# Optimization experiments

Hardware: AMD Instinct MI355X
Metric: run time of the kernel (lower is better)

Reference implementation:

```python
import jax, jax.numpy as jnp
import numpy as np

N_NODES = 50000


def setup_inputs() -> dict:
    key = jax.random.key(0)
    ks = jax.random.split(key, 8)
    d_in, d_h, d_out = 128, 128, 1
    s_in = 1.0 / np.sqrt(d_in)
    s_h = 1.0 / np.sqrt(d_h)
    return {
        "x": jax.random.normal(ks[0], (N_NODES, d_in), dtype=jnp.float32),
        "edge_index": jax.random.randint(ks[1], (2, 800000), 0, N_NODES, dtype=jnp.int64),
        "W1a": jax.random.normal(ks[2], (d_in, d_h), dtype=jnp.float32) * s_in,
        "b1a": jnp.zeros((d_h,), dtype=jnp.float32),
        "W1b": jax.random.normal(ks[3], (d_h, d_h), dtype=jnp.float32) * s_h,
        "b1b": jnp.zeros((d_h,), dtype=jnp.float32),
        "W2a": jax.random.normal(ks[4], (d_h, d_h), dtype=jnp.float32) * s_h,
        "b2a": jnp.zeros((d_h,), dtype=jnp.float32),
        "W2b": jax.random.normal(ks[5], (d_h, d_h), dtype=jnp.float32) * s_h,
        "b2b": jnp.zeros((d_h,), dtype=jnp.float32),
        "Wfc": jax.random.normal(ks[6], (d_h, d_out), dtype=jnp.float32) * s_h,
        "bfc": jnp.zeros((d_out,), dtype=jnp.float32),
    }


def _gin_conv(x, src, dst, Wa, ba, Wb, bb):
    # GINConv (eps=0): h_i = MLP((1+eps)*x_i + sum_{j->i} x_j)
    agg = jax.ops.segment_sum(x[src], dst, num_segments=N_NODES)
    h = x + agg
    h = jax.nn.relu(h @ Wa + ba)
    h = jax.nn.relu(h @ Wb + bb)
    return h


def reference(x, edge_index, W1a, b1a, W1b, b1b, W2a, b2a, W2b, b2b, Wfc, bfc):
    src, dst = edge_index[0], edge_index[1]
    h = _gin_conv(x, src, dst, W1a, b1a, W1b, b1b)
    h = _gin_conv(h, src, dst, W2a, b2a, W2b, b2b)
    out = h @ Wfc + bfc
    return jax.nn.sigmoid(out)
```

## Files before the change

### kernel.cpp

```cpp
#include <hip/hip_runtime.h>
#include <hip/hip_fp16.h>
#include <cstdint>
#include <cstddef>

#define D 128
#define NP 8
#define S_CSR 96
typedef __attribute__((ext_vector_type(8))) _Float16 half8;
typedef __attribute__((ext_vector_type(4))) float f32x4;
typedef __attribute__((ext_vector_type(4))) uint uint4n;

__device__ __forceinline__ uint pack2h(float x, float y) {
    __half2 h = __floats2half2_rn(x, y);
    return *(uint*)&h;
}
__device__ __forceinline__ __half2 u2h(uint u) { return *(__half2*)&u; }
__device__ __forceinline__ uint h2u(__half2 h) { return *(uint*)&h; }
__device__ __forceinline__ int pad16(int v) { return (v + 15) & ~15; }

__global__ __launch_bounds__(256) void prep(const float* __restrict__ x,
                                            uint* __restrict__ X32,
                                            const float* __restrict__ W0,
                                            const float* __restrict__ W1,
                                            const float* __restrict__ W2,
                                            const float* __restrict__ W3,
                                            ushort* __restrict__ P0,
                                            ushort* __restrict__ P1,
                                            ushort* __restrict__ P2,
                                            ushort* __restrict__ P3,
                                            int* __restrict__ cnt,
                                            const unsigned int* __restrict__ ei,
                                            int* __restrict__ flag,
                                            uint* __restrict__ zrow0,
                                            uint* __restrict__ zrow2,
                                            ushort* __restrict__ csr,
                                            int M, int cvtB, int mB) {
    int b = blockIdx.x, t = threadIdx.x;
    if (b < cvtB) {
        long long gid = (long long)b * 256 + t;
        if (gid >= (long long)M * 16) return;
        int node = (int)(gid >> 4), q = (int)(gid & 15);
        const float4* xp = (const float4*)(x + (size_t)node * D + q * 8);
        float4 v0 = xp[0], v1 = xp[1];
        uint4n o;
        o.x = pack2h(v0.x, v0.y); o.y = pack2h(v0.z, v0.w);
        o.z = pack2h(v1.x, v1.y); o.w = pack2h(v1.z, v1.w);
        ((uint4n*)X32)[(size_t)node * 16 + q] = o;
    } else if (b < cvtB + 256) {
        int o = ((b - cvtB) & 63) * 256 + t;
        int which = (b - cvtB) >> 6;
        const float* W = which == 0 ? W0 : which == 1 ? W1 : which == 2 ? W2 : W3;
        ushort* P = which == 0 ? P0 : which == 1 ? P1 : which == 2 ? P2 : P3;
        int j = o & 7, g = (o >> 3) & 3, n = (o >> 5) & 127, ks = o >> 12;
        int k = ks * 32 + g * 8 + j;
        __half h = __float2half_rn(W[k * 128 + n]);
        P[o] = *(ushort*)&h;
    } else if (b < cvtB + 256 + mB) {
        int i = (b - cvtB - 256) * 256 + t;
        if (i < M) cnt[i] = 0;
        if (b == cvtB + 256 && t < 64) {
            zrow0[(size_t)M * 64 + t] = 0u;
            zrow2[(size_t)M * 64 + t] = 0u;
            if (t == 0) {
                int is64 = (ei[1] == 0u && ei[3] == 0u && ei[5] == 0u && ei[7] == 0u) ? 1 : 0;
                *flag = is64;
            }
        }
    } else {
        long long idx = (long long)(b - cvtB - 256 - mB) * 256 + t;
        long long tot = (long long)M * (S_CSR / 2);
        uint sv = (uint)M | ((uint)M << 16);
        if (idx < tot) ((uint*)csr)[idx] = sv;
    }
}

__global__ __launch_bounds__(256) void fill_csr_part(const void* __restrict__ ei,
                                                     const int* __restrict__ flag,
                                                     int* __restrict__ cnt,
                                                     ushort* __restrict__ csr,
                                                     int E, int M, int nslice) {
    int p = blockIdx.x & (NP - 1);
    int slice = blockIdx.x >> 3;
    int psz = (M + NP - 1) / NP;
    int lo = p * psz, hi = min(M, lo + psz);
    int eps = (E + nslice - 1) / nslice;
    int e0 = slice * eps, e1 = min(E, e0 + eps);
    int sh = *flag;
    const int* sp = (const int*)ei;
    const int* dp = sp + ((long long)E << sh);
    for (int e = e0 + threadIdx.x; e < e1; e += 256) {
        int d = dp[e << sh];
        if (d >= lo && d < hi) {
            int s = sp[e << sh];
            int pos = atomicAdd(&cnt[d], 1);
            if (pos < S_CSR) csr[(size_t)d * S_CSR + pos] = (ushort)s;
        }
    }
}

__global__ __launch_bounds__(256) void aggregate_f16(const uint* __restrict__ X,
                                                     const int* __restrict__ cnt,
                                                     const ushort* __restrict__ csr,
                                                     uint* __restrict__ H, int M) {
    int wv = __builtin_amdgcn_readfirstlane((int)(threadIdx.x >> 6));
    int node = blockIdx.x * 4 + wv;
    if (node >= M) return;
    int lane = threadIdx.x & 63;

    int degp = min(pad16(__builtin_amdgcn_readfirstlane(cnt[node])), S_CSR);
    const ushort* ep = csr + (size_t)node * S_CSR;

    __half2 acc = u2h(X[(size_t)node * 64 + lane]);
    for (int j0 = 0; j0 < degp; j0 += 16) {
        uint4n i0 = *(const uint4n*)(ep + j0);
        uint4n i1 = *(const uint4n*)(ep + j0 + 8);
        uint us[16];
        us[0]  = X[(size_t)(i0.x & 0xffff) * 64 + lane];
        us[1]  = X[(size_t)(i0.x >> 16)    * 64 + lane];
        us[2]  = X[(size_t)(i0.y & 0xffff) * 64 + lane];
        us[3]  = X[(size_t)(i0.y >> 16)    * 64 + lane];
        us[4]  = X[(size_t)(i0.z & 0xffff) * 64 + lane];
        us[5]  = X[(size_t)(i0.z >> 16)    * 64 + lane];
        us[6]  = X[(size_t)(i0.w & 0xffff) * 64 + lane];
        us[7]  = X[(size_t)(i0.w >> 16)    * 64 + lane];
        us[8]  = X[(size_t)(i1.x & 0xffff) * 64 + lane];
        us[9]  = X[(size_t)(i1.x >> 16)    * 64 + lane];
        us[10] = X[(size_t)(i1.y & 0xffff) * 64 + lane];
        us[11] = X[(size_t)(i1.y >> 16)    * 64 + lane];
        us[12] = X[(size_t)(i1.z & 0xffff) * 64 + lane];
        us[13] = X[(size_t)(i1.z >> 16)    * 64 + lane];
        us[14] = X[(size_t)(i1.w & 0xffff) * 64 + lane];
        us[15] = X[(size_t)(i1.w >> 16)    * 64 + lane];
        __half2 t0 = __hadd2(__hadd2(u2h(us[0]), u2h(us[1])), __hadd2(u2h(us[2]), u2h(us[3])));
        __half2 t1 = __hadd2(__hadd2(u2h(us[4]), u2h(us[5])), __hadd2(u2h(us[6]), u2h(us[7])));
        __half2 t2 = __hadd2(__hadd2(u2h(us[8]), u2h(us[9])), __hadd2(u2h(us[10]), u2h(us[11])));
        __half2 t3 = __hadd2(__hadd2(u2h(us[12]), u2h(us[13])), __hadd2(u2h(us[14]), u2h(us[15])));
        acc = __hadd2(acc, __hadd2(__hadd2(t0, t1), __hadd2(t2, t3)));
    }
    __builtin_nontemporal_store(h2u(acc), &H[(size_t)node * 64 + lane]);
}

template <int FINAL>
__global__ __launch_bounds__(256) void mlp_mfma(const ushort* __restrict__ A,
                                                const ushort* __restrict__ Bpa,
                                                const float* __restrict__ ba,
                                                const ushort* __restrict__ Bpb,
                                                const float* __restrict__ bb,
                                                const float* __restrict__ Wfc,
                                                const float* __restrict__ bfc,
                                                ushort* __restrict__ C,
                                                float* __restrict__ out,
                                                int M, int nTiles) {
    __shared__ ushort sB[2][16384];
    __shared__ ushort Hs[4][16][16][8];
    int t = threadIdx.x;
    int wv = t >> 6, lane = t & 63;
    int l15 = lane & 15, g = lane >> 4;

    for (int i = t; i < 2048; i += 256) {
        ((uint4n*)sB[0])[i] = ((const uint4n*)Bpa)[i];
        ((uint4n*)sB[1])[i] = ((const uint4n*)Bpb)[i];
    }
    __syncthreads();

    float bva[8], bvb[8], wf[8];
#pragma unroll
    for (int nt = 0; nt < 8; ++nt) {
        bva[nt] = ba[nt * 16 + l15];
        bvb[nt] = bb[nt * 16 + l15];
        if (FINAL) wf[nt] = Wfc[nt * 16 + l15];
    }
    float bf = FINAL ? bfc[0] : 0.f;

    for (int tile = blockIdx.x; tile < nTiles; tile += gridDim.x) {
        int rb = tile * 64 + wv * 16;
        int arow = rb + l15;
        int arow_c = arow < M ? arow : M - 1;

        half8 a_frag[4];
        const uint4n* ap = (const uint4n*)(A + (size_t)arow_c * D + g * 8);
#pragma unroll
        for (int ks = 0; ks < 4; ++ks) {
            uint4n u = __builtin_nontemporal_load(ap + ks * 4);
            a_frag[ks] = *(half8*)&u;
        }

        f32x4 acc[8];
#pragma unroll
        for (int i = 0; i < 8; ++i) acc[i] = (f32x4){0.f, 0.f, 0.f, 0.f};
#pragma unroll
        for (int ks = 0; ks < 4; ++ks) {
#pragma unroll
            for (int nt = 0; nt < 8; ++nt) {
                half8 b = *(const half8*)&sB[0][((ks * 128 + nt * 16 + l15) * 4 + g) << 3];
                acc[nt] = __builtin_amdgcn_mfma_f32_16x16x32_f16(a_frag[ks], b, acc[nt], 0, 0, 0);
            }
        }
#pragma unroll
        for (int nt = 0; nt < 8; ++nt) {
            int col = nt * 16 + l15;
            int u = col >> 3, j = col & 7;
#pragma unroll
            for (int r = 0; r < 4; ++r) {
                int row = g * 4 + r;
                float v = fmaxf(acc[nt][r] + bva[nt], 0.f);
                __half hh = __float2half_rn(v);
                Hs[wv][row][u ^ row][j] = *(ushort*)&hh;
            }
        }

        f32x4 acc2[8];
#pragma unroll
        for (int i = 0; i < 8; ++i) acc2[i] = (f32x4){0.f, 0.f, 0.f, 0.f};
#pragma unroll
        for (int ks = 0; ks < 4; ++ks) {
            half8 a = *(const half8*)&Hs[wv][l15][(ks * 4 + g) ^ l15][0];
#pragma unroll
            for (int nt = 0; nt < 8; ++nt) {
                half8 b = *(const half8*)&sB[1][((ks * 128 + nt * 16 + l15) * 4 + g) << 3];
                acc2[nt] = __builtin_amdgcn_mfma_f32_16x16x32_f16(a, b, acc2[nt], 0, 0, 0);
            }
        }

        if (!FINAL) {
#pragma unroll
            for (int nt = 0; nt < 8; ++nt) {
                int col = nt * 16 + l15;
#pragma unroll
                for (int r = 0; r < 4; ++r) {
                    int row = rb + g * 4 + r;
                    if (row < M) {
                        float v = fmaxf(acc2[nt][r] + bvb[nt], 0.f);
                        __half hh = __float2half_rn(v);
                        C[(size_t)row * D + col] = *(ushort*)&hh;
                    }
                }
            }
        } else {
            float p[4] = {0.f, 0.f, 0.f, 0.f};
#pragma unroll
            for (int nt = 0; nt < 8; ++nt) {
#pragma unroll
                for (int r = 0; r < 4; ++r) {
                    float v = fmaxf(acc2[nt][r] + bvb[nt], 0.f);
                    p[r] = fmaf(v, wf[nt], p[r]);
                }
            }
#pragma unroll
            for (int r = 0; r < 4; ++r) {
                p[r] += __shfl_xor(p[r], 1);
                p[r] += __shfl_xor(p[r], 2);
                p[r] += __shfl_xor(p[r], 4);
                p[r] += __shfl_xor(p[r], 8);
            }
            if (l15 == 0) {
#pragma unroll
                for (int r = 0; r < 4; ++r) {
                    int row = rb + g * 4 + r;
                    if (row < M) out[row] = 1.f / (1.f + expf(-(p[r] + bf)));
                }
            }
        }
    }
}

extern "C" void kernel_launch(void* const* d_in, const int* in_sizes, int n_in,
                              void* d_out, int out_size, void* d_ws, size_t ws_size,
                              hipStream_t stream) {
    const float* x   = (const float*)d_in[0];
    const void*  ei  = d_in[1];
    const float* W1a = (const float*)d_in[2];
    const float* b1a = (const float*)d_in[3];
    const float* W1b = (const float*)d_in[4];
    const float* b1b = (const float*)d_in[5];
    const float* W2a = (const float*)d_in[6];
    const float* b2a = (const float*)d_in[7];
    const float* W2b = (const float*)d_in[8];
    const float* b2b = (const float*)d_in[9];
    const float* Wfc = (const float*)d_in[10];
    const float* bfc = (const float*)d_in[11];
    float* out = (float*)d_out;

    int M = in_sizes[0] / D;
    int E = in_sizes[1] / 2;
    size_t nf2 = (size_t)(M + 1) * D;

    ushort* B0 = (ushort*)d_ws;
    ushort* B1 = B0 + nf2;
    ushort* B2 = B1 + nf2;
    ushort* P1a = B2 + nf2;
    ushort* P1b = P1a + 16384;
    ushort* P2a = P1b + 16384;
    ushort* P2b = P2a + 16384;
    int* cnt    = (int*)(P2b + 16384);
    ushort* csr = (ushort*)(cnt + M);
    int* flag   = (int*)(csr + (size_t)M * S_CSR);

    int mBlocks = (M + 255) / 256;
    int cvtB = (M * 16 + 255) / 256;
    int csrB = (int)(((long long)M * (S_CSR / 2) + 255) / 256);
    int aggBlocks = (M + 3) / 4;
    int nTiles = (M + 63) / 64;
    int nslice = 256;

    prep<<<cvtB + 256 + mBlocks + csrB, 256, 0, stream>>>(
        x, (uint*)B0, W1a, W1b, W2a, W2b, P1a, P1b, P2a, P2b,
        cnt, (const unsigned int*)ei, flag, (uint*)B0, (uint*)B2, csr,
        M, cvtB, mBlocks);

    fill_csr_part<<<NP * nslice, 256, 0, stream>>>(ei, flag, cnt, csr, E, M, nslice);

    aggregate_f16<<<aggBlocks, 256, 0, stream>>>((const uint*)B0, cnt, csr, (uint*)B1, M);
    mlp_mfma<0><<<512, 256, 0, stream>>>(B1, P1a, b1a, P1b, b1b, nullptr, nullptr, B2, nullptr, M, nTiles);

    aggregate_f16<<<aggBlocks, 256, 0, stream>>>((const uint*)B2, cnt, csr, (uint*)B0, M);
    mlp_mfma<1><<<512, 256, 0, stream>>>(B0, P2a, b2a, P2b, b2b, Wfc, bfc, nullptr, out, M, nTiles);
}
```

Measured before the change: 141.8 us.

## Build CSR via per-block destination buckets instead of repeated partition scans

Replaces the CSR fill, which scanned every edge once per destination partition, with a two-pass scheme. The first pass reads each edge once and writes packed (src,dst) pairs into per-block shared-memory-counted buckets. The second pass fills each partition's CSR rows from its buckets. It also drops the full sentinel memset of the CSR array and instead pads only each row's tail up to the next multiple of 16. This adds an extra kernel and bucket storage, relies on a fixed per-bucket capacity, and packs dst into 16 bits.

```diff
diff --git a/kernel.cpp b/kernel.cpp
--- a/kernel.cpp
+++ b/kernel.cpp
@@ -6,6 +6,8 @@
 #define D 128
 #define NP 8
 #define S_CSR 96
+#define BK_EDGES 4096
+#define CAP_PB 768
 typedef __attribute__((ext_vector_type(8))) _Float16 half8;
 typedef __attribute__((ext_vector_type(4))) float f32x4;
 typedef __attribute__((ext_vector_type(4))) uint uint4n;
@@ -33,7 +35,6 @@
                                             int* __restrict__ flag,
                                             uint* __restrict__ zrow0,
                                             uint* __restrict__ zrow2,
-                                            ushort* __restrict__ csr,
                                             int M, int cvtB, int mB) {
     int b = blockIdx.x, t = threadIdx.x;
     if (b < cvtB) {
@@ -55,7 +56,7 @@
         int k = ks * 32 + g * 8 + j;
         __half h = __float2half_rn(W[k * 128 + n]);
         P[o] = *(ushort*)&h;
-    } else if (b < cvtB + 256 + mB) {
+    } else {
         int i = (b - cvtB - 256) * 256 + t;
         if (i < M) cnt[i] = 0;
         if (b == cvtB + 256 && t < 64) {
@@ -66,36 +67,61 @@
                 *flag = is64;
             }
         }
-    } else {
-        long long idx = (long long)(b - cvtB - 256 - mB) * 256 + t;
-        long long tot = (long long)M * (S_CSR / 2);
-        uint sv = (uint)M | ((uint)M << 16);
-        if (idx < tot) ((uint*)csr)[idx] = sv;
-    }
-}
-
-__global__ __launch_bounds__(256) void fill_csr_part(const void* __restrict__ ei,
-                                                     const int* __restrict__ flag,
-                                                     int* __restrict__ cnt,
-                                                     ushort* __restrict__ csr,
-                                                     int E, int M, int nslice) {
-    int p = blockIdx.x & (NP - 1);
-    int slice = blockIdx.x >> 3;
-    int psz = (M + NP - 1) / NP;
-    int lo = p * psz, hi = min(M, lo + psz);
-    int eps = (E + nslice - 1) / nslice;
-    int e0 = slice * eps, e1 = min(E, e0 + eps);
+    }
+}
+
+__global__ __launch_bounds__(256) void bucket_edges(const void* __restrict__ ei,
+                                                    const int* __restrict__ flag,
+                                                    uint* __restrict__ bkt,
+                                                    int* __restrict__ bcnt,
+                                                    int E, float inv_psz) {
+    __shared__ int lcnt[NP];
+    int t = threadIdx.x;
+    if (t < NP) lcnt[t] = 0;
+    __syncthreads();
     int sh = *flag;
     const int* sp = (const int*)ei;
     const int* dp = sp + ((long long)E << sh);
-    for (int e = e0 + threadIdx.x; e < e1; e += 256) {
-        int d = dp[e << sh];
-        if (d >= lo && d < hi) {
-            int s = sp[e << sh];
+    int e0 = blockIdx.x * BK_EDGES;
+    int e1 = min(E, e0 + BK_EDGES);
+    uint* myreg = bkt + (size_t)blockIdx.x * NP * CAP_PB;
+    for (int e = e0 + t; e < e1; e += 256) {
+        int d = dp[(long long)e << sh];
+        int s = sp[(long long)e << sh];
+        int b = min(NP - 1, (int)((float)d * inv_psz));
+        int pos = atomicAdd(&lcnt[b], 1);
+        if (pos < CAP_PB) myreg[b * CAP_PB + pos] = (uint)s | ((uint)d << 16);
+    }
+    __syncthreads();
+    if (t < NP) bcnt[blockIdx.x * NP + t] = min(lcnt[t], CAP_PB);
+}
+
+__global__ __launch_bounds__(256) void fill_from_buckets(const uint* __restrict__ bkt,
+                                                         const int* __restrict__ bcnt,
+                                                         int* __restrict__ cnt,
+                                                         ushort* __restrict__ csr,
+                                                         int nBlk, int ns) {
+    int p = blockIdx.x & (NP - 1);
+    int q = blockIdx.x >> 3;
+    for (int blk = q; blk < nBlk; blk += ns) {
+        int n = bcnt[blk * NP + p];
+        const uint* base = bkt + ((size_t)blk * NP + p) * CAP_PB;
+        for (int i = threadIdx.x; i < n; i += 256) {
+            uint u = base[i];
+            int d = (int)(u >> 16), s = (int)(u & 0xffffu);
             int pos = atomicAdd(&cnt[d], 1);
             if (pos < S_CSR) csr[(size_t)d * S_CSR + pos] = (ushort)s;
         }
     }
+}
+
+__global__ __launch_bounds__(256) void pad_tail(const int* __restrict__ cnt,
+                                                ushort* __restrict__ csr, int M) {
+    int i = blockIdx.x * 256 + threadIdx.x;
+    if (i >= M) return;
+    int deg = min(cnt[i], S_CSR);
+    int degp = min(pad16(deg), S_CSR);
+    for (int j = deg; j < degp; ++j) csr[(size_t)i * S_CSR + j] = (ushort)M;
 }
 
 __global__ __launch_bounds__(256) void aggregate_f16(const uint* __restrict__ X,
@@ -284,6 +310,7 @@
     int M = in_sizes[0] / D;
     int E = in_sizes[1] / 2;
     size_t nf2 = (size_t)(M + 1) * D;
+    int nBlkB = (E + BK_EDGES - 1) / BK_EDGES;
 
     ushort* B0 = (ushort*)d_ws;
     ushort* B1 = B0 + nf2;
@@ -295,20 +322,24 @@
     int* cnt    = (int*)(P2b + 16384);
     ushort* csr = (ushort*)(cnt + M);
     int* flag   = (int*)(csr + (size_t)M * S_CSR);
+    int* bcnt   = flag + 2;
+    uint* bkt   = (uint*)(bcnt + (size_t)nBlkB * NP);
 
     int mBlocks = (M + 255) / 256;
     int cvtB = (M * 16 + 255) / 256;
-    int csrB = (int)(((long long)M * (S_CSR / 2) + 255) / 256);
     int aggBlocks = (M + 3) / 4;
     int nTiles = (M + 63) / 64;
-    int nslice = 256;
-
-    prep<<<cvtB + 256 + mBlocks + csrB, 256, 0, stream>>>(
+    int psz = (M + NP - 1) / NP;
+    float inv_psz = 1.0f / (float)psz;
+    int ns = 64;
+
+    prep<<<cvtB + 256 + mBlocks, 256, 0, stream>>>(
         x, (uint*)B0, W1a, W1b, W2a, W2b, P1a, P1b, P2a, P2b,
-        cnt, (const unsigned int*)ei, flag, (uint*)B0, (uint*)B2, csr,
-        M, cvtB, mBlocks);
-
-    fill_csr_part<<<NP * nslice, 256, 0, stream>>>(ei, flag, cnt, csr, E, M, nslice);
+        cnt, (const unsigned int*)ei, flag, (uint*)B0, (uint*)B2, M, cvtB, mBlocks);
+
+    bucket_edges<<<nBlkB, 256, 0, stream>>>(ei, flag, bkt, bcnt, E, inv_psz);
+    fill_from_buckets<<<NP * ns, 256, 0, stream>>>(bkt, bcnt, cnt, csr, nBlkB, ns);
+    pad_tail<<<mBlocks, 256, 0, stream>>>(cnt, csr, M);
 
     aggregate_f16<<<aggBlocks, 256, 0, stream>>>((const uint*)B0, cnt, csr, (uint*)B1, M);
     mlp_mfma<0><<<512, 256, 0, stream>>>(B1, P1a, b1a, P1b, b1b, nullptr, nullptr, B2, nullptr, M, nTiles);
```

Result: slower. 151.4 us (+6.8%).
